# Kernel tuning notes

Measured on AMD Instinct MI355X. Metric: run time of the kernel, lower is better.

The kernel has to match this reference:

```python
import jax, jax.numpy as jnp
import numpy as np

NUM_QUBITS = 12
ENC_COPIES = 1
ANSATZ_COPIES = 2
BATCH = 1024
NUM_THETAS = NUM_QUBITS * (ANSATZ_COPIES + 1) * 2  # 72

_H = jnp.asarray(np.array([[1.0, 1.0], [1.0, -1.0]], np.complex64) / np.sqrt(2.0))


def _apply_1q(state, U, q):
    # state: [B, 2, 2, ..., 2] (n qubit axes); apply 2x2 unitary U on qubit q
    s = jnp.moveaxis(state, 1 + q, -1)
    s = jnp.einsum('...j,ij->...i', s, U)
    return jnp.moveaxis(s, -1, 1 + q)


def _apply_zpow(state, t, q):
    # cirq Z**t = diag(1, e^{i*pi*t}); t is scalar or per-batch [B]
    n = state.ndim - 1
    phase = jnp.exp(1j * jnp.pi * t).astype(jnp.complex64)
    factor = jnp.stack([jnp.ones_like(phase), phase], axis=-1)
    if factor.ndim == 2:  # batched exponent -> broadcast over other qubit axes
        factor = factor.reshape((factor.shape[0],) + (1,) * (n - 1) + (2,))
    s = jnp.moveaxis(state, 1 + q, -1)
    return jnp.moveaxis(s * factor, -1, 1 + q)


def _ypow_unitary(t):
    # cirq Y**t up to global phase e^{i*pi*t/2} (irrelevant for Z expectations)
    a = 0.5 * jnp.pi * t
    c, s = jnp.cos(a), jnp.sin(a)
    return jnp.stack([jnp.stack([c, -s]), jnp.stack([s, c])]).astype(jnp.complex64)


def _apply_cnot(state, c, t):
    s = jnp.moveaxis(state, (1 + c, 1 + t), (-2, -1))
    s = jnp.stack([s[..., 0, :], s[..., 1, ::-1]], axis=-2)
    return jnp.moveaxis(s, (-2, -1), (1 + c, 1 + t))


def _encoding_block(state, x):
    # FirstOrderPauliZEncoding: per copy, per qubit: H then Z**x_q
    for _ in range(ENC_COPIES):
        for q in range(NUM_QUBITS):
            state = _apply_1q(state, _H, q)
            state = _apply_zpow(state, x[:, q], q)
    return state


def _ansatz_block(state, th, with_cnot):
    # EfficientSU2 layer: Y**th[q,0], Z**th[q,1] per qubit, then CNOT chain
    for q in range(NUM_QUBITS):
        state = _apply_1q(state, _ypow_unitary(th[q, 0]), q)
        state = _apply_zpow(state, th[q, 1], q)
    if with_cnot:
        for q in range(NUM_QUBITS - 1):
            state = _apply_cnot(state, q, q + 1)
    return state


_enc = jax.checkpoint(_encoding_block)
_ans_cnot = jax.checkpoint(lambda st, th: _ansatz_block(st, th, True))
_ans_last = jax.checkpoint(lambda st, th: _ansatz_block(st, th, False))


def _circuit(inputs, thetas):
    b = inputs.shape[0]
    state = jnp.zeros((b, 2 ** NUM_QUBITS), jnp.complex64).at[:, 0].set(1.0)
    state = state.reshape((b,) + (2,) * NUM_QUBITS)
    state = _enc(state, inputs)
    th = thetas.reshape(ANSATZ_COPIES + 1, NUM_QUBITS, 2)
    for l in range(ANSATZ_COPIES + 1):
        state = (_ans_cnot if l < ANSATZ_COPIES else _ans_last)(state, th[l])
    # readouts: <Z_q> for each qubit
    probs = state.real ** 2 + state.imag ** 2
    exps = []
    for q in range(NUM_QUBITS):
        axes = tuple(a for a in range(1, NUM_QUBITS + 1) if a != 1 + q)
        p = probs.sum(axis=axes)  # [B, 2]
        exps.append(p[:, 0] - p[:, 1])
    return jnp.stack(exps, axis=-1)  # [B, NUM_QUBITS]


def setup_inputs() -> dict:
    key = jax.random.key(0)
    k1, k2 = jax.random.split(key)
    inputs = jax.random.uniform(k1, (BATCH, NUM_QUBITS), jnp.float32)
    thetas = jax.random.uniform(k2, (NUM_THETAS,), jnp.float32, minval=-1.0, maxval=1.0)
    return {"inputs": inputs, "thetas": thetas}


def reference(inputs, thetas):
    return _circuit(inputs, thetas)
```

## Files before the change

kernel.cpp:

```cpp
#include <hip/hip_runtime.h>


#define PI_F 3.14159265358979323846f
#define NR 32
#define PAD 66

__device__ __forceinline__ float2 cmul(float2 a, float2 b) {
    return make_float2(a.x*b.x - a.y*b.y, a.x*b.y + a.y*b.x);
}
__device__ __forceinline__ float2 cmulc(float2 a, float2 b) {
    return make_float2(a.x*b.x + a.y*b.y, a.y*b.x - a.x*b.y);
}

template<int RB>
__device__ __forceinline__ void ypow_reg(float2 (&a)[NR], float c, float s) {
    #pragma unroll
    for (int r0 = 0; r0 < NR; ++r0) {
        if ((r0 >> RB) & 1) continue;
        const int r1 = r0 | (1 << RB);
        float2 a0 = a[r0], a1 = a[r1];
        a[r0] = make_float2(c*a0.x - s*a1.x, c*a0.y - s*a1.y);
        a[r1] = make_float2(s*a0.x + c*a1.x, s*a0.y + c*a1.y);
    }
}

__device__ __forceinline__ void exchange_AB(float2 (&a)[NR], float2* buf,
                                            int w, int lane, float c6, float s6) {
    float2* wb = buf + w * (NR * PAD);
    __syncthreads();
    #pragma unroll
    for (int r = 0; r < NR; ++r)
        wb[r * PAD + (lane & 31) * 2 + (lane >> 5)] = a[r];
    __syncthreads();
    const int g = lane >> 1;
    const float k0 = (lane & 1) ? s6 : c6;
    const float k1 = (lane & 1) ? c6 : -s6;
    #pragma unroll
    for (int r = 0; r < NR; ++r) {
        float2 p0 = wb[g * PAD + r * 2];
        float2 p1 = wb[g * PAD + r * 2 + 1];
        a[r] = make_float2(k0*p0.x + k1*p1.x, k0*p0.y + k1*p1.y);
    }
}

__device__ __forceinline__ void exchange_BA(float2 (&a)[NR], float2* buf,
                                            int w, int lane, float c0, float s0) {
    __syncthreads();
    const int p6w = lane ^ (w << 5);
    #pragma unroll
    for (int r = 0; r < NR; ++r)
        buf[p6w * PAD + r * 2 + w] = a[r];
    __syncthreads();
    const float k0 = w ? s0 : c0;
    const float k1 = w ? c0 : -s0;
    #pragma unroll
    for (int rp = 0; rp < NR; ++rp) {
        const int ylow = (rp << 6) | lane;
        const int t = ylow ^ (ylow >> 1);
        const int base = (t >> 5) * PAD + (t & 31) * 2;
        float2 p0 = buf[base];
        float2 p1 = buf[base + 1];
        a[rp] = make_float2(k0*p0.x + k1*p1.x, k0*p0.y + k1*p1.y);
    }
}

__device__ __forceinline__ void ypow_block_regA(float2 (&a)[NR], const float* __restrict__ th) {
    { float s,c; __sincosf(0.5f*PI_F*th[2],  &s,&c); ypow_reg<4>(a,c,s); }
    { float s,c; __sincosf(0.5f*PI_F*th[4],  &s,&c); ypow_reg<3>(a,c,s); }
    { float s,c; __sincosf(0.5f*PI_F*th[6],  &s,&c); ypow_reg<2>(a,c,s); }
    { float s,c; __sincosf(0.5f*PI_F*th[8],  &s,&c); ypow_reg<1>(a,c,s); }
    { float s,c; __sincosf(0.5f*PI_F*th[10], &s,&c); ypow_reg<0>(a,c,s); }
}
__device__ __forceinline__ void ypow_block_regB(float2 (&a)[NR], const float* __restrict__ th) {
    { float s,c; __sincosf(0.5f*PI_F*th[14], &s,&c); ypow_reg<4>(a,c,s); }
    { float s,c; __sincosf(0.5f*PI_F*th[16], &s,&c); ypow_reg<3>(a,c,s); }
    { float s,c; __sincosf(0.5f*PI_F*th[18], &s,&c); ypow_reg<2>(a,c,s); }
    { float s,c; __sincosf(0.5f*PI_F*th[20], &s,&c); ypow_reg<1>(a,c,s); }
    { float s,c; __sincosf(0.5f*PI_F*th[22], &s,&c); ypow_reg<0>(a,c,s); }
}

__device__ __forceinline__ void fused_z_B(float2 (&a)[NR], int w, int lane,
                                          const float* __restrict__ th) {
    float alpha = w ? th[1] : 0.0f;
    #pragma unroll
    for (int k = 0; k < 6; ++k)
        alpha += ((lane >> k) & 1) ? th[2*(6-k)+1] : 0.0f;
    float2 zb; __sincosf(PI_F * alpha, &zb.y, &zb.x);
    float2 zq[5];
    #pragma unroll
    for (int j = 0; j < 5; ++j)
        __sincosf(PI_F * th[2*(11-j)+1], &zq[j].y, &zq[j].x);
    float2 cur = zb;
    a[0] = cmul(a[0], cur);
    #pragma unroll
    for (int k = 1; k < NR; ++k) {
        const int bit = __builtin_ctz(k);
        const int g = k ^ (k >> 1);
        cur = ((g >> bit) & 1) ? cmul(cur, zq[bit]) : cmulc(cur, zq[bit]);
        a[g] = cmul(a[g], cur);
    }
}

__global__ __launch_bounds__(128) void vqc_kernel(
    const float* __restrict__ inputs,
    const float* __restrict__ thetas,
    float* __restrict__ out)
{
    __shared__ __align__(16) float2 buf[64 * PAD];
    __shared__ float redBuf[24];

    const int b = blockIdx.x;
    const int tid = threadIdx.x;
    const int w = tid >> 6;
    const int lane = tid & 63;
    const float* x = inputs + b * 12;

    float2 a[NR];

    float phb = 0.0f;
    #pragma unroll
    for (int k = 0; k < 6; ++k)
        phb += ((lane >> k) & 1) ? x[11 - k] : 0.0f;
    float2 cisb; __sincosf(PI_F * phb, &cisb.y, &cisb.x);
    float2 E;    __sincosf(PI_F * x[0], &E.y, &E.x);
    float s0, c0; __sincosf(0.5f * PI_F * thetas[0], &s0, &c0);
    float2 Fw = w ? make_float2(s0 + c0 * E.x,  c0 * E.y)
                  : make_float2(c0 - s0 * E.x, -s0 * E.y);
    float2 g0 = cmul(Fw, cisb);
    g0.x *= 0.015625f; g0.y *= 0.015625f;
    float2 zr[5];
    #pragma unroll
    for (int j = 0; j < 5; ++j)
        __sincosf(PI_F * x[5 - j], &zr[j].y, &zr[j].x);
    {
        float2 cur = g0;
        a[0] = cur;
        #pragma unroll
        for (int k = 1; k < NR; ++k) {
            const int bit = __builtin_ctz(k);
            const int g = k ^ (k >> 1);
            cur = ((g >> bit) & 1) ? cmul(cur, zr[bit]) : cmulc(cur, zr[bit]);
            a[g] = cur;
        }
    }

    const float* th0 = thetas;
    const float* th1 = thetas + 24;
    const float* th2 = thetas + 48;

    ypow_block_regA(a, th0);
    { float s,c; __sincosf(0.5f*PI_F*th0[12], &s,&c); exchange_AB(a, buf, w, lane, c, s); }
    ypow_block_regB(a, th0);
    fused_z_B(a, w, lane, th0);
    { float s,c; __sincosf(0.5f*PI_F*th1[0],  &s,&c); exchange_BA(a, buf, w, lane, c, s); }

    ypow_block_regA(a, th1);
    { float s,c; __sincosf(0.5f*PI_F*th1[12], &s,&c); exchange_AB(a, buf, w, lane, c, s); }
    ypow_block_regB(a, th1);
    fused_z_B(a, w, lane, th1);
    { float s,c; __sincosf(0.5f*PI_F*th2[0],  &s,&c); exchange_BA(a, buf, w, lane, c, s); }

    ypow_block_regA(a, th2);
    { float s,c; __sincosf(0.5f*PI_F*th2[12], &s,&c); exchange_AB(a, buf, w, lane, c, s); }
    ypow_block_regB(a, th2);

    float totalP = 0.0f;
    float D[5] = {0, 0, 0, 0, 0};
    #pragma unroll
    for (int r = 0; r < NR; ++r) {
        const float p = a[r].x * a[r].x + a[r].y * a[r].y;
        totalP += p;
        #pragma unroll
        for (int j = 0; j < 5; ++j)
            D[j] += ((r >> j) & 1) ? -p : p;
    }
    #pragma unroll
    for (int q = 0; q < 12; ++q) {
        float v;
        if (q == 0)       v = w ? -totalP : totalP;
        else if (q <= 6)  v = ((lane >> (6 - q)) & 1) ? -totalP : totalP;
        else              v = D[11 - q];
        #pragma unroll
        for (int off = 32; off >= 1; off >>= 1)
            v += __shfl_xor(v, off, 64);
        if (lane == 0) redBuf[w * 12 + q] = v;
    }
    __syncthreads();
    if (tid < 12) out[b * 12 + tid] = redBuf[tid] + redBuf[12 + tid];
}

extern "C" void kernel_launch(void* const* d_in, const int* in_sizes, int n_in,
                              void* d_out, int out_size, void* d_ws, size_t ws_size,
                              hipStream_t stream) {
    const float* inputs = (const float*)d_in[0];
    const float* thetas = (const float*)d_in[1];
    float* out = (float*)d_out;
    vqc_kernel<<<dim3(1024), dim3(128), 0, stream>>>(inputs, thetas, out);
}
```

Before: 78.01 us.

## Precompute gate sincos table in LDS, vectorize complex math, use DPP reductions

Computes all Y-rotation and Z-phase sin/cos values once per block into a shared table instead of every thread recomputing them. Switches complex arithmetic to ext_vector float2 types so packed math can be used. In the exchange stage it drops the leading sync and replaces the middle block barrier with a wave-local lgkmcnt wait, which is valid because each wave uses its own buffer region. The final reduction now uses DPP and ds_swizzle lane exchanges instead of generic shuffles. The costs are an extra block barrier at the start and the correctness risk of relying on wave-local ordering without a full barrier.

Measured after the change: 74.64 us. 4.3% less time.

```diff
diff --git a/kernel.cpp b/kernel.cpp
--- a/kernel.cpp
+++ b/kernel.cpp
@@ -5,45 +5,83 @@
 #define NR 32
 #define PAD 66
 
-__device__ __forceinline__ float2 cmul(float2 a, float2 b) {
-    return make_float2(a.x*b.x - a.y*b.y, a.x*b.y + a.y*b.x);
-}
-__device__ __forceinline__ float2 cmulc(float2 a, float2 b) {
-    return make_float2(a.x*b.x + a.y*b.y, a.y*b.x - a.x*b.y);
+typedef __attribute__((ext_vector_type(2))) float v2f;
+
+__device__ __forceinline__ v2f mkv(float x, float y) { v2f r; r.x = x; r.y = y; return r; }
+__device__ __forceinline__ v2f cmul(v2f a, v2f b) {
+    return a.x * b + a.y * mkv(-b.y, b.x);
+}
+__device__ __forceinline__ v2f cmulc(v2f a, v2f b) {
+    return a.x * mkv(b.x, -b.y) + a.y * mkv(b.y, b.x);
+}
+
+template<int M>
+__device__ __forceinline__ float lane_xor_f(float v) {
+    if constexpr (M == 1) {
+        return __int_as_float(__builtin_amdgcn_update_dpp(
+            0, __float_as_int(v), 0xB1, 0xF, 0xF, false));
+    } else if constexpr (M == 2) {
+        return __int_as_float(__builtin_amdgcn_update_dpp(
+            0, __float_as_int(v), 0x4E, 0xF, 0xF, false));
+    } else if constexpr (M == 4) {
+        return __int_as_float(__builtin_amdgcn_ds_swizzle(__float_as_int(v), 0x101F));
+    } else if constexpr (M == 8) {
+        return __int_as_float(__builtin_amdgcn_ds_swizzle(__float_as_int(v), 0x201F));
+    } else if constexpr (M == 16) {
+        return __int_as_float(__builtin_amdgcn_ds_swizzle(__float_as_int(v), 0x401F));
+    } else {
+        return __shfl_xor(v, 32, 64);
+    }
 }
 
 template<int RB>
-__device__ __forceinline__ void ypow_reg(float2 (&a)[NR], float c, float s) {
+__device__ __forceinline__ void ypow_reg(v2f (&a)[NR], float c, float s) {
     #pragma unroll
     for (int r0 = 0; r0 < NR; ++r0) {
         if ((r0 >> RB) & 1) continue;
         const int r1 = r0 | (1 << RB);
-        float2 a0 = a[r0], a1 = a[r1];
-        a[r0] = make_float2(c*a0.x - s*a1.x, c*a0.y - s*a1.y);
-        a[r1] = make_float2(s*a0.x + c*a1.x, s*a0.y + c*a1.y);
-    }
-}
-
-__device__ __forceinline__ void exchange_AB(float2 (&a)[NR], float2* buf,
+        v2f a0 = a[r0], a1 = a[r1];
+        a[r0] = c * a0 - s * a1;
+        a[r1] = s * a0 + c * a1;
+    }
+}
+
+__device__ __forceinline__ void ypowA(v2f (&a)[NR], const v2f* __restrict__ yt) {
+    { v2f t = yt[1]; ypow_reg<4>(a, t.x, t.y); }
+    { v2f t = yt[2]; ypow_reg<3>(a, t.x, t.y); }
+    { v2f t = yt[3]; ypow_reg<2>(a, t.x, t.y); }
+    { v2f t = yt[4]; ypow_reg<1>(a, t.x, t.y); }
+    { v2f t = yt[5]; ypow_reg<0>(a, t.x, t.y); }
+}
+__device__ __forceinline__ void ypowB(v2f (&a)[NR], const v2f* __restrict__ yt) {
+    { v2f t = yt[7];  ypow_reg<4>(a, t.x, t.y); }
+    { v2f t = yt[8];  ypow_reg<3>(a, t.x, t.y); }
+    { v2f t = yt[9];  ypow_reg<2>(a, t.x, t.y); }
+    { v2f t = yt[10]; ypow_reg<1>(a, t.x, t.y); }
+    { v2f t = yt[11]; ypow_reg<0>(a, t.x, t.y); }
+}
+
+template<bool PRE_SYNC>
+__device__ __forceinline__ void exchange_AB(v2f (&a)[NR], v2f* buf,
                                             int w, int lane, float c6, float s6) {
-    float2* wb = buf + w * (NR * PAD);
-    __syncthreads();
+    v2f* wb = buf + w * (NR * PAD);
+    if (PRE_SYNC) __syncthreads();
     #pragma unroll
     for (int r = 0; r < NR; ++r)
         wb[r * PAD + (lane & 31) * 2 + (lane >> 5)] = a[r];
-    __syncthreads();
+    asm volatile("s_waitcnt lgkmcnt(0)" ::: "memory");
     const int g = lane >> 1;
     const float k0 = (lane & 1) ? s6 : c6;
     const float k1 = (lane & 1) ? c6 : -s6;
     #pragma unroll
     for (int r = 0; r < NR; ++r) {
-        float2 p0 = wb[g * PAD + r * 2];
-        float2 p1 = wb[g * PAD + r * 2 + 1];
-        a[r] = make_float2(k0*p0.x + k1*p1.x, k0*p0.y + k1*p1.y);
-    }
-}
-
-__device__ __forceinline__ void exchange_BA(float2 (&a)[NR], float2* buf,
+        v2f p0 = wb[g * PAD + r * 2];
+        v2f p1 = wb[g * PAD + r * 2 + 1];
+        a[r] = k0 * p0 + k1 * p1;
+    }
+}
+
+__device__ __forceinline__ void exchange_BA(v2f (&a)[NR], v2f* buf,
                                             int w, int lane, float c0, float s0) {
     __syncthreads();
     const int p6w = lane ^ (w << 5);
@@ -58,39 +96,24 @@
         const int ylow = (rp << 6) | lane;
         const int t = ylow ^ (ylow >> 1);
         const int base = (t >> 5) * PAD + (t & 31) * 2;
-        float2 p0 = buf[base];
-        float2 p1 = buf[base + 1];
-        a[rp] = make_float2(k0*p0.x + k1*p1.x, k0*p0.y + k1*p1.y);
-    }
-}
-
-__device__ __forceinline__ void ypow_block_regA(float2 (&a)[NR], const float* __restrict__ th) {
-    { float s,c; __sincosf(0.5f*PI_F*th[2],  &s,&c); ypow_reg<4>(a,c,s); }
-    { float s,c; __sincosf(0.5f*PI_F*th[4],  &s,&c); ypow_reg<3>(a,c,s); }
-    { float s,c; __sincosf(0.5f*PI_F*th[6],  &s,&c); ypow_reg<2>(a,c,s); }
-    { float s,c; __sincosf(0.5f*PI_F*th[8],  &s,&c); ypow_reg<1>(a,c,s); }
-    { float s,c; __sincosf(0.5f*PI_F*th[10], &s,&c); ypow_reg<0>(a,c,s); }
-}
-__device__ __forceinline__ void ypow_block_regB(float2 (&a)[NR], const float* __restrict__ th) {
-    { float s,c; __sincosf(0.5f*PI_F*th[14], &s,&c); ypow_reg<4>(a,c,s); }
-    { float s,c; __sincosf(0.5f*PI_F*th[16], &s,&c); ypow_reg<3>(a,c,s); }
-    { float s,c; __sincosf(0.5f*PI_F*th[18], &s,&c); ypow_reg<2>(a,c,s); }
-    { float s,c; __sincosf(0.5f*PI_F*th[20], &s,&c); ypow_reg<1>(a,c,s); }
-    { float s,c; __sincosf(0.5f*PI_F*th[22], &s,&c); ypow_reg<0>(a,c,s); }
-}
-
-__device__ __forceinline__ void fused_z_B(float2 (&a)[NR], int w, int lane,
-                                          const float* __restrict__ th) {
+        v2f p0 = buf[base];
+        v2f p1 = buf[base + 1];
+        a[rp] = k0 * p0 + k1 * p1;
+    }
+}
+
+__device__ __forceinline__ void fused_z_B(v2f (&a)[NR], int w, int lane,
+                                          const float* __restrict__ th,
+                                          const v2f* __restrict__ zt) {
     float alpha = w ? th[1] : 0.0f;
     #pragma unroll
     for (int k = 0; k < 6; ++k)
         alpha += ((lane >> k) & 1) ? th[2*(6-k)+1] : 0.0f;
-    float2 zb; __sincosf(PI_F * alpha, &zb.y, &zb.x);
-    float2 zq[5];
-    #pragma unroll
-    for (int j = 0; j < 5; ++j)
-        __sincosf(PI_F * th[2*(11-j)+1], &zq[j].y, &zq[j].x);
-    float2 cur = zb;
+    float zs, zc; __sincosf(PI_F * alpha, &zs, &zc);
+    v2f zq[5];
+    #pragma unroll
+    for (int j = 0; j < 5; ++j) zq[j] = zt[j];
+    v2f cur = mkv(zc, zs);
     a[0] = cmul(a[0], cur);
     #pragma unroll
     for (int k = 1; k < NR; ++k) {
@@ -106,7 +129,8 @@
     const float* __restrict__ thetas,
     float* __restrict__ out)
 {
-    __shared__ __align__(16) float2 buf[64 * PAD];
+    __shared__ __align__(16) v2f buf[64 * PAD];
+    __shared__ v2f thTab[46];
     __shared__ float redBuf[24];
 
     const int b = blockIdx.x;
@@ -115,25 +139,38 @@
     const int lane = tid & 63;
     const float* x = inputs + b * 12;
 
-    float2 a[NR];
+    if (tid < 36) {
+        const int l = tid / 12, q = tid % 12;
+        float s, c; __sincosf(0.5f * PI_F * thetas[l * 24 + 2 * q], &s, &c);
+        thTab[tid] = mkv(c, s);
+    } else if (tid < 46) {
+        const int j = tid - 36, l = j / 5, jj = j % 5;
+        float s, c; __sincosf(PI_F * thetas[l * 24 + 2 * (11 - jj) + 1], &s, &c);
+        thTab[tid] = mkv(c, s);
+    }
 
     float phb = 0.0f;
     #pragma unroll
     for (int k = 0; k < 6; ++k)
         phb += ((lane >> k) & 1) ? x[11 - k] : 0.0f;
-    float2 cisb; __sincosf(PI_F * phb, &cisb.y, &cisb.x);
-    float2 E;    __sincosf(PI_F * x[0], &E.y, &E.x);
-    float s0, c0; __sincosf(0.5f * PI_F * thetas[0], &s0, &c0);
-    float2 Fw = w ? make_float2(s0 + c0 * E.x,  c0 * E.y)
-                  : make_float2(c0 - s0 * E.x, -s0 * E.y);
-    float2 g0 = cmul(Fw, cisb);
-    g0.x *= 0.015625f; g0.y *= 0.015625f;
-    float2 zr[5];
-    #pragma unroll
-    for (int j = 0; j < 5; ++j)
-        __sincosf(PI_F * x[5 - j], &zr[j].y, &zr[j].x);
+    float cbs, cbc; __sincosf(PI_F * phb, &cbs, &cbc);
+    v2f cisb = mkv(cbc, cbs);
+    float es, ec; __sincosf(PI_F * x[0], &es, &ec);
+    v2f zr[5];
+    #pragma unroll
+    for (int j = 0; j < 5; ++j) {
+        float ss, cc; __sincosf(PI_F * x[5 - j], &ss, &cc);
+        zr[j] = mkv(cc, ss);
+    }
+
+    __syncthreads();
+
+    v2f a[NR];
     {
-        float2 cur = g0;
+        v2f t0 = thTab[0];
+        v2f Fw = w ? mkv(t0.y + t0.x * ec,  t0.x * es)
+                   : mkv(t0.x - t0.y * ec, -t0.y * es);
+        v2f cur = cmul(Fw, cisb) * 0.015625f;
         a[0] = cur;
         #pragma unroll
         for (int k = 1; k < NR; ++k) {
@@ -144,25 +181,21 @@
         }
     }
 
-    const float* th0 = thetas;
-    const float* th1 = thetas + 24;
-    const float* th2 = thetas + 48;
-
-    ypow_block_regA(a, th0);
-    { float s,c; __sincosf(0.5f*PI_F*th0[12], &s,&c); exchange_AB(a, buf, w, lane, c, s); }
-    ypow_block_regB(a, th0);
-    fused_z_B(a, w, lane, th0);
-    { float s,c; __sincosf(0.5f*PI_F*th1[0],  &s,&c); exchange_BA(a, buf, w, lane, c, s); }
-
-    ypow_block_regA(a, th1);
-    { float s,c; __sincosf(0.5f*PI_F*th1[12], &s,&c); exchange_AB(a, buf, w, lane, c, s); }
-    ypow_block_regB(a, th1);
-    fused_z_B(a, w, lane, th1);
-    { float s,c; __sincosf(0.5f*PI_F*th2[0],  &s,&c); exchange_BA(a, buf, w, lane, c, s); }
-
-    ypow_block_regA(a, th2);
-    { float s,c; __sincosf(0.5f*PI_F*th2[12], &s,&c); exchange_AB(a, buf, w, lane, c, s); }
-    ypow_block_regB(a, th2);
+    ypowA(a, &thTab[0]);
+    { v2f t = thTab[6];  exchange_AB<false>(a, buf, w, lane, t.x, t.y); }
+    ypowB(a, &thTab[0]);
+    fused_z_B(a, w, lane, thetas, &thTab[36]);
+    { v2f t = thTab[12]; exchange_BA(a, buf, w, lane, t.x, t.y); }
+
+    ypowA(a, &thTab[12]);
+    { v2f t = thTab[18]; exchange_AB<true>(a, buf, w, lane, t.x, t.y); }
+    ypowB(a, &thTab[12]);
+    fused_z_B(a, w, lane, thetas + 24, &thTab[41]);
+    { v2f t = thTab[24]; exchange_BA(a, buf, w, lane, t.x, t.y); }
+
+    ypowA(a, &thTab[24]);
+    { v2f t = thTab[30]; exchange_AB<true>(a, buf, w, lane, t.x, t.y); }
+    ypowB(a, &thTab[24]);
 
     float totalP = 0.0f;
     float D[5] = {0, 0, 0, 0, 0};
@@ -180,9 +213,12 @@
         if (q == 0)       v = w ? -totalP : totalP;
         else if (q <= 6)  v = ((lane >> (6 - q)) & 1) ? -totalP : totalP;
         else              v = D[11 - q];
-        #pragma unroll
-        for (int off = 32; off >= 1; off >>= 1)
-            v += __shfl_xor(v, off, 64);
+        v += lane_xor_f<32>(v);
+        v += lane_xor_f<16>(v);
+        v += lane_xor_f<8>(v);
+        v += lane_xor_f<4>(v);
+        v += lane_xor_f<2>(v);
+        v += lane_xor_f<1>(v);
         if (lane == 0) redBuf[w * 12 + q] = v;
     }
     __syncthreads();
```
